# Kernel optimization log

Measured on AMD Instinct MI355X. Metric: run time of the kernel, lower is better.

Reference implementation:

```python
import jax, jax.numpy as jnp
import numpy as np

N = 10000      # nodes (= num_spatial_nodes)
E = 320000     # edges
IN = 4         # in_channels
HID = 256      # hidden_channels
H1, C1 = 4, 64 # conv1: heads, per-head out (hidden//heads)
EDIM = 1       # edge_feature_size
EPS = 1e-5


def _layernorm(x, g, b):
    mu = jnp.mean(x, axis=-1, keepdims=True)
    var = jnp.mean(jnp.square(x - mu), axis=-1, keepdims=True)
    return (x - mu) / jnp.sqrt(var + EPS) * g + b


def _gatv2(x, src, dst, ea, Wl, bl, Wr, br, We, att, bias, H, C, n):
    # PyG GATv2Conv: lin_l on source, lin_r on target, lin_edge on edge_attr
    xl = (x @ Wl + bl).reshape(n, H, C)
    xr = (x @ Wr + br).reshape(n, H, C)
    ee = (ea @ We).reshape(-1, H, C)
    m = jax.nn.leaky_relu(xl[src] + xr[dst] + ee, 0.2)   # [E', H, C]
    logit = jnp.einsum('ehc,hc->eh', m, att)             # [E', H]
    # segment softmax over incoming edges of each dst node
    mx = jax.ops.segment_max(logit, dst, num_segments=n)
    ex = jnp.exp(logit - mx[dst])
    den = jax.ops.segment_sum(ex, dst, num_segments=n)
    alpha = ex / den[dst]
    out = jax.ops.segment_sum(xl[src] * alpha[:, :, None], dst, num_segments=n)
    return out.reshape(n, H * C) + bias


def setup_inputs() -> dict:
    key = jax.random.key(0)
    ks = jax.random.split(key, 32)
    gl = lambda k, shape, fan: (jax.random.normal(k, shape, jnp.float32) / np.sqrt(fan)).astype(jnp.float32)
    inp = {}
    inp['x'] = jax.random.normal(ks[0], (N, IN), jnp.float32)
    inp['edge_index'] = jax.random.randint(ks[1], (2, E), 0, N, jnp.int32)
    inp['edge_attr'] = jax.random.normal(ks[2], (E, EDIM), jnp.float32)
    # conv1 (heads=4, out=64, concat -> 256)
    inp['Wl1'] = gl(ks[3], (IN, HID), IN);  inp['bl1'] = jnp.zeros((HID,), jnp.float32)
    inp['Wr1'] = gl(ks[4], (IN, HID), IN);  inp['br1'] = jnp.zeros((HID,), jnp.float32)
    inp['We1'] = gl(ks[5], (EDIM, HID), EDIM)
    inp['att1'] = gl(ks[6], (H1, C1), C1)
    inp['bias1'] = jnp.zeros((HID,), jnp.float32)
    inp['g1'] = jnp.ones((HID,), jnp.float32); inp['be1'] = jnp.zeros((HID,), jnp.float32)
    # conv2 (heads=1, out=256)
    inp['Wl2'] = gl(ks[7], (HID, HID), HID); inp['bl2'] = jnp.zeros((HID,), jnp.float32)
    inp['Wr2'] = gl(ks[8], (HID, HID), HID); inp['br2'] = jnp.zeros((HID,), jnp.float32)
    inp['We2'] = gl(ks[9], (EDIM, HID), EDIM)
    inp['att2'] = gl(ks[10], (1, HID), HID)
    inp['bias2'] = jnp.zeros((HID,), jnp.float32)
    inp['g2'] = jnp.ones((HID,), jnp.float32); inp['be2'] = jnp.zeros((HID,), jnp.float32)
    # policy head
    inp['Wp1'] = gl(ks[11], (HID, HID // 2), HID); inp['bp1'] = jnp.zeros((HID // 2,), jnp.float32)
    inp['Wp2'] = gl(ks[12], (HID // 2, IN), HID // 2); inp['bp2'] = jnp.zeros((IN,), jnp.float32)
    return inp


def reference(x, edge_index, edge_attr,
              Wl1, bl1, Wr1, br1, We1, att1, bias1, g1, be1,
              Wl2, bl2, Wr2, br2, We2, att2, bias2, g2, be2,
              Wp1, bp1, Wp2, bp2):
    src, dst = edge_index[0], edge_index[1]
    # add_self_loops with fill_value='mean': loop edge_attr = mean of incoming edge_attr
    deg = jax.ops.segment_sum(jnp.ones((E,), jnp.float32), dst, num_segments=N)
    loop_attr = jax.ops.segment_sum(edge_attr, dst, num_segments=N) / jnp.maximum(deg, 1.0)[:, None]
    ar = jnp.arange(N, dtype=src.dtype)
    src_a = jnp.concatenate([src, ar]); dst_a = jnp.concatenate([dst, ar])
    ea_a = jnp.concatenate([edge_attr, loop_attr], axis=0)
    h = _gatv2(x, src_a, dst_a, ea_a, Wl1, bl1, Wr1, br1, We1, att1, bias1, H1, C1, N)
    h = jax.nn.relu(_layernorm(h, g1, be1))
    h = _gatv2(h, src_a, dst_a, ea_a, Wl2, bl2, Wr2, br2, We2, att2, bias2, 1, HID, N)
    h = jax.nn.relu(_layernorm(h, g2, be2))
    logits = jax.nn.relu(h @ Wp1 + bp1) @ Wp2 + bp2   # [N, IN]
    return jax.nn.softmax(logits.reshape(1, -1), axis=1)
```

## Files before the change

### kernel.cpp

```cpp
#include <hip/hip_runtime.h>
#include <math.h>

#define N_NODES 10000
#define N_EDGES 320000
#define N_AUG   (N_EDGES + N_NODES)
#define CPK_CAP 330752
#define HID     256

typedef short short8 __attribute__((ext_vector_type(8)));
typedef float floatx16 __attribute__((ext_vector_type(16)));

static __device__ __forceinline__ unsigned bf16rne(float f) {
  unsigned u = __float_as_uint(f);
  return (u + 0x7FFFu + ((u >> 16) & 1u)) >> 16;
}

__global__ void k_deg(const int* __restrict__ dst, const float* __restrict__ ea,
                      int* __restrict__ deg, float* __restrict__ asum,
                      int* __restrict__ rank) {
  int e = blockIdx.x * blockDim.x + threadIdx.x;
  if (e < N_EDGES) {
    int d = dst[e];
    rank[e] = atomicAdd(&deg[d], 1);
    atomicAdd(&asum[d], ea[e]);
  }
}

__global__ void __launch_bounds__(256) k_scan(
    const int* __restrict__ deg, const float* __restrict__ asum,
    int* __restrict__ offs, float* __restrict__ lattr) {
  __shared__ int wsum[4];
  int t = threadIdx.x;
  int base = t * 40;
  int s = 0;
  for (int i = 0; i < 40; i++) {
    int n = base + i;
    if (n < N_NODES) s += deg[n] + 1;
  }
  int v = s;
  #pragma unroll
  for (int d = 1; d < 64; d <<= 1) {
    int u = __shfl_up(v, d);
    if ((t & 63) >= d) v += u;
  }
  if ((t & 63) == 63) wsum[t >> 6] = v;
  __syncthreads();
  int wb = 0;
  for (int i = 0; i < (t >> 6); i++) wb += wsum[i];
  int run = wb + v - s;
  for (int i = 0; i < 40; i++) {
    int n = base + i;
    if (n < N_NODES) {
      offs[n] = run;
      int d = deg[n];
      run += d + 1;
      lattr[n] = asum[n] / (float)max(d, 1);
    }
  }
  if (t == 255) offs[N_NODES] = wb + v;
}

__global__ void k_scatter(const int* __restrict__ src, const int* __restrict__ dst,
                          const float* __restrict__ ea, const float* __restrict__ lattr,
                          const int* __restrict__ offs, const int* __restrict__ rank,
                          int2* __restrict__ cpk) {
  int e = blockIdx.x * blockDim.x + threadIdx.x;
  if (e >= N_AUG) {
    if (e < CPK_CAP) cpk[e] = make_int2(0, 0);
    return;
  }
  int pos, s; float a;
  if (e < N_EDGES) {
    s = src[e];
    int d = dst[e];
    a = ea[e];
    pos = offs[d] + rank[e];
  } else {
    s = e - N_EDGES;
    a = lattr[s];
    pos = offs[s + 1] - 1;
  }
  cpk[pos] = make_int2(s, __float_as_int(a));
}

__global__ void __launch_bounds__(256) k_prep(
    const float* __restrict__ W1, const float* __restrict__ W2,
    const float* __restrict__ Wp1,
    unsigned short* __restrict__ Wt, unsigned short* __restrict__ Wp1t) {
  __shared__ float tile[32][33];
  int z = blockIdx.z;
  int kb = blockIdx.x * 32, nb = blockIdx.y * 32;
  int t = threadIdx.x;
  int tx = t & 31, ty = t >> 5;
  if (z < 2) {
    const float* W = z ? W2 : W1;
    int rowoff = z * 256;
    #pragma unroll
    for (int rep = 0; rep < 4; rep++)
      tile[ty + 8*rep][tx] = W[(kb + ty + 8*rep)*HID + nb + tx];
    __syncthreads();
    #pragma unroll
    for (int rep = 0; rep < 4; rep++) {
      int n = nb + ty + 8*rep;
      Wt[(rowoff + n)*256 + kb + tx] = (unsigned short)bf16rne(tile[tx][ty + 8*rep]);
    }
  } else {
    if (nb >= 128) return;
    #pragma unroll
    for (int rep = 0; rep < 4; rep++)
      tile[ty + 8*rep][tx] = Wp1[(kb + ty + 8*rep)*128 + nb + tx];
    __syncthreads();
    #pragma unroll
    for (int rep = 0; rep < 4; rep++) {
      int n = nb + ty + 8*rep;
      Wp1t[n*256 + kb + tx] = (unsigned short)bf16rne(tile[tx][ty + 8*rep]);
    }
  }
}

#define C1_EDGE(xs, av, l0, l1, l2, l3, p)                                              \
  {                                                                                     \
    l0 = fmaf(xs.x,wl0.x, fmaf(xs.y,wl1.x, fmaf(xs.z,wl2.x, fmaf(xs.w,wl3.x, blv.x)))); \
    l1 = fmaf(xs.x,wl0.y, fmaf(xs.y,wl1.y, fmaf(xs.z,wl2.y, fmaf(xs.w,wl3.y, blv.y)))); \
    l2 = fmaf(xs.x,wl0.z, fmaf(xs.y,wl1.z, fmaf(xs.z,wl2.z, fmaf(xs.w,wl3.z, blv.z)))); \
    l3 = fmaf(xs.x,wl0.w, fmaf(xs.y,wl1.w, fmaf(xs.z,wl2.w, fmaf(xs.w,wl3.w, blv.w)))); \
    float m0 = l0 + fmaf(av, we.x, r4.x); m0 = fmaxf(m0, 0.2f*m0);                      \
    float m1 = l1 + fmaf(av, we.y, r4.y); m1 = fmaxf(m1, 0.2f*m1);                      \
    float m2 = l2 + fmaf(av, we.z, r4.z); m2 = fmaxf(m2, 0.2f*m2);                      \
    float m3 = l3 + fmaf(av, we.w, r4.w); m3 = fmaxf(m3, 0.2f*m3);                      \
    p = m0*at.x + m1*at.y + m2*at.z + m3*at.w;                                          \
  }

#define C1_BODY8()                                                              \
  {                                                                             \
    float avA = __int_as_float(eA.y), avB = __int_as_float(eB.y);               \
    float avC = __int_as_float(eC.y), avD = __int_as_float(eD.y);               \
    float avE = __int_as_float(eE.y), avF = __int_as_float(eF.y);               \
    float avG = __int_as_float(eG.y), avH = __int_as_float(eH.y);               \
    float lA0,lA1,lA2,lA3,pA, lB0,lB1,lB2,lB3,pB;                               \
    float lC0,lC1,lC2,lC3,pC, lD0,lD1,lD2,lD3,pD;                               \
    float lE0,lE1,lE2,lE3,pE, lF0,lF1,lF2,lF3,pF;                               \
    float lG0,lG1,lG2,lG3,pG, lH0,lH1,lH2,lH3,pH;                               \
    C1_EDGE(xA, avA, lA0,lA1,lA2,lA3, pA);                                      \
    C1_EDGE(xB, avB, lB0,lB1,lB2,lB3, pB);                                      \
    C1_EDGE(xC, avC, lC0,lC1,lC2,lC3, pC);                                      \
    C1_EDGE(xD, avD, lD0,lD1,lD2,lD3, pD);                                      \
    C1_EDGE(xE, avE, lE0,lE1,lE2,lE3, pE);                                      \
    C1_EDGE(xF, avF, lF0,lF1,lF2,lF3, pF);                                      \
    C1_EDGE(xG, avG, lG0,lG1,lG2,lG3, pG);                                      \
    C1_EDGE(xH, avH, lH0,lH1,lH2,lH3, pH);                                      \
    float sAB = b1 ? pA : pB, kAB = b1 ? pB : pA;                               \
    float qAB = kAB + __shfl_xor(sAB, 1);                                       \
    float sCD = b1 ? pC : pD, kCD = b1 ? pD : pC;                               \
    float qCD = kCD + __shfl_xor(sCD, 1);                                       \
    float sEF = b1 ? pE : pF, kEF = b1 ? pF : pE;                               \
    float qEF = kEF + __shfl_xor(sEF, 1);                                       \
    float sGH = b1 ? pG : pH, kGH = b1 ? pH : pG;                               \
    float qGH = kGH + __shfl_xor(sGH, 1);                                       \
    float u0s = b2 ? qAB : qCD, u0k = b2 ? qCD : qAB;                           \
    float u0 = u0k + __shfl_xor(u0s, 2);                                        \
    float u1s = b2 ? qEF : qGH, u1k = b2 ? qGH : qEF;                           \
    float u1 = u1k + __shfl_xor(u1s, 2);                                        \
    float vvs = b4 ? u0 : u1, vvk = b4 ? u1 : u0;                               \
    float vv = vvk + __shfl_xor(vvs, 4);                                        \
    vv += __shfl_xor(vv, 8);                                                    \
    float exv = expf(vv);                                                       \
    float xAe = __shfl(exv, 0, 16), xBe = __shfl(exv, 1, 16);                   \
    float xCe = __shfl(exv, 2, 16), xDe = __shfl(exv, 3, 16);                   \
    float xEe = __shfl(exv, 4, 16), xFe = __shfl(exv, 5, 16);                   \
    float xGe = __shfl(exv, 6, 16), xHe = __shfl(exv, 7, 16);                   \
    D += ((xAe + xBe) + (xCe + xDe)) + ((xEe + xFe) + (xGe + xHe));             \
    a0 = fmaf(xDe, lD0, fmaf(xCe, lC0, fmaf(xBe, lB0, fmaf(xAe, lA0, a0))));    \
    a0 = fmaf(xHe, lH0, fmaf(xGe, lG0, fmaf(xFe, lF0, fmaf(xEe, lE0, a0))));    \
    a1 = fmaf(xDe, lD1, fmaf(xCe, lC1, fmaf(xBe, lB1, fmaf(xAe, lA1, a1))));    \
    a1 = fmaf(xHe, lH1, fmaf(xGe, lG1, fmaf(xFe, lF1, fmaf(xEe, lE1, a1))));    \
    a2 = fmaf(xDe, lD2, fmaf(xCe, lC2, fmaf(xBe, lB2, fmaf(xAe, lA2, a2))));    \
    a2 = fmaf(xHe, lH2, fmaf(xGe, lG2, fmaf(xFe, lF2, fmaf(xEe, lE2, a2))));    \
    a3 = fmaf(xDe, lD3, fmaf(xCe, lC3, fmaf(xBe, lB3, fmaf(xAe, lA3, a3))));    \
    a3 = fmaf(xHe, lH3, fmaf(xGe, lG3, fmaf(xFe, lF3, fmaf(xEe, lE3, a3))));    \
  }

__global__ void __launch_bounds__(256) k_conv1(
    const float* __restrict__ x,
    const float* __restrict__ Wl, const float* __restrict__ bl,
    const float* __restrict__ Wr, const float* __restrict__ br,
    const float* __restrict__ We, const float* __restrict__ att,
    const int* __restrict__ offs, const int2* __restrict__ cpk,
    const float* __restrict__ bias, const float* __restrict__ g,
    const float* __restrict__ be, uint2* __restrict__ h1b) {
  int t = threadIdx.x;
  int n = blockIdx.x * 4 + (t >> 6);
  int c = 4 * (t & 63);
  bool b1 = (t & 1) != 0, b2 = (t & 2) != 0, b4 = (t & 4) != 0;

  float4 wl0 = *(const float4*)&Wl[0*HID + c];
  float4 wl1 = *(const float4*)&Wl[1*HID + c];
  float4 wl2 = *(const float4*)&Wl[2*HID + c];
  float4 wl3 = *(const float4*)&Wl[3*HID + c];
  float4 blv = *(const float4*)&bl[c];
  float4 we  = *(const float4*)&We[c];
  float4 at  = *(const float4*)&att[c];

  float4 xn = *(const float4*)&x[n*4];
  float4 r4;
  {
    float4 wr0 = *(const float4*)&Wr[0*HID + c];
    float4 wr1 = *(const float4*)&Wr[1*HID + c];
    float4 wr2 = *(const float4*)&Wr[2*HID + c];
    float4 wr3 = *(const float4*)&Wr[3*HID + c];
    float4 brv = *(const float4*)&br[c];
    r4.x = fmaf(xn.x,wr0.x, fmaf(xn.y,wr1.x, fmaf(xn.z,wr2.x, fmaf(xn.w,wr3.x, brv.x))));
    r4.y = fmaf(xn.x,wr0.y, fmaf(xn.y,wr1.y, fmaf(xn.z,wr2.y, fmaf(xn.w,wr3.y, brv.y))));
    r4.z = fmaf(xn.x,wr0.z, fmaf(xn.y,wr1.z, fmaf(xn.z,wr2.z, fmaf(xn.w,wr3.z, brv.z))));
    r4.w = fmaf(xn.x,wr0.w, fmaf(xn.y,wr1.w, fmaf(xn.z,wr2.w, fmaf(xn.w,wr3.w, brv.w))));
  }

  int js = __builtin_amdgcn_readfirstlane(offs[n]);
  int je = __builtin_amdgcn_readfirstlane(offs[n+1]);

  float D = 0.f, a0 = 0.f, a1 = 0.f, a2 = 0.f, a3 = 0.f;

  int j = js;
  if (je - js >= 16) {
    int2 eA = cpk[j],   eB = cpk[j+1], eC = cpk[j+2], eD = cpk[j+3];
    int2 eE = cpk[j+4], eF = cpk[j+5], eG = cpk[j+6], eH = cpk[j+7];
    int2 fA = cpk[j+8],  fB = cpk[j+9],  fC = cpk[j+10], fD = cpk[j+11];
    int2 fE = cpk[j+12], fF = cpk[j+13], fG = cpk[j+14], fH = cpk[j+15];
    float4 xA = *(const float4*)&x[eA.x*4];
    float4 xB = *(const float4*)&x[eB.x*4];
    float4 xC = *(const float4*)&x[eC.x*4];
    float4 xD = *(const float4*)&x[eD.x*4];
    float4 xE = *(const float4*)&x[eE.x*4];
    float4 xF = *(const float4*)&x[eF.x*4];
    float4 xG = *(const float4*)&x[eG.x*4];
    float4 xH = *(const float4*)&x[eH.x*4];
    for (; j + 15 < je; j += 8) {
      float4 yA = *(const float4*)&x[fA.x*4];
      float4 yB = *(const float4*)&x[fB.x*4];
      float4 yC = *(const float4*)&x[fC.x*4];
      float4 yD = *(const float4*)&x[fD.x*4];
      float4 yE = *(const float4*)&x[fE.x*4];
      float4 yF = *(const float4*)&x[fF.x*4];
      float4 yG = *(const float4*)&x[fG.x*4];
      float4 yH = *(const float4*)&x[fH.x*4];
      int2 gA = cpk[j+16], gB = cpk[j+17], gC = cpk[j+18], gD = cpk[j+19];
      int2 gE = cpk[j+20], gF = cpk[j+21], gG = cpk[j+22], gH = cpk[j+23];
      C1_BODY8();
      eA = fA; eB = fB; eC = fC; eD = fD; eE = fE; eF = fF; eG = fG; eH = fH;
      fA = gA; fB = gB; fC = gC; fD = gD; fE = gE; fF = gF; fG = gG; fH = gH;
      xA = yA; xB = yB; xC = yC; xD = yD; xE = yE; xF = yF; xG = yG; xH = yH;
    }
    C1_BODY8();
    j += 8;
  }
  for (; j + 7 < je; j += 8) {
    int2 eA = cpk[j],   eB = cpk[j+1], eC = cpk[j+2], eD = cpk[j+3];
    int2 eE = cpk[j+4], eF = cpk[j+5], eG = cpk[j+6], eH = cpk[j+7];
    float4 xA = *(const float4*)&x[eA.x*4];
    float4 xB = *(const float4*)&x[eB.x*4];
    float4 xC = *(const float4*)&x[eC.x*4];
    float4 xD = *(const float4*)&x[eD.x*4];
    float4 xE = *(const float4*)&x[eE.x*4];
    float4 xF = *(const float4*)&x[eF.x*4];
    float4 xG = *(const float4*)&x[eG.x*4];
    float4 xH = *(const float4*)&x[eH.x*4];
    C1_BODY8();
  }
  for (; j < je; j++) {
    int2 eA = cpk[j];
    float4 xA = *(const float4*)&x[eA.x*4];
    float avA = __int_as_float(eA.y);
    float lA0,lA1,lA2,lA3,pA;
    C1_EDGE(xA, avA, lA0,lA1,lA2,lA3, pA);
    #pragma unroll
    for (int msk = 1; msk < 16; msk <<= 1) pA += __shfl_xor(pA, msk);
    float eAx = expf(pA);
    D += eAx;
    a0 = fmaf(eAx, lA0, a0);
    a1 = fmaf(eAx, lA1, a1);
    a2 = fmaf(eAx, lA2, a2);
    a3 = fmaf(eAx, lA3, a3);
  }

  float inv = 1.f / D;
  float4 b4v = *(const float4*)&bias[c];
  float o0 = fmaf(a0, inv, b4v.x);
  float o1 = fmaf(a1, inv, b4v.y);
  float o2 = fmaf(a2, inv, b4v.z);
  float o3 = fmaf(a3, inv, b4v.w);

  float s = o0 + o1 + o2 + o3;
  #pragma unroll
  for (int msk = 1; msk < 64; msk <<= 1) s += __shfl_xor(s, msk);
  float mu = s * (1.f / 256.f);
  float d0 = o0 - mu, d1 = o1 - mu, d2 = o2 - mu, d3 = o3 - mu;
  float sq = d0*d0 + d1*d1 + d2*d2 + d3*d3;
  #pragma unroll
  for (int msk = 1; msk < 64; msk <<= 1) sq += __shfl_xor(sq, msk);
  float rstd = rsqrtf(sq * (1.f / 256.f) + 1e-5f);
  float4 g4  = *(const float4*)&g[c];
  float4 be4 = *(const float4*)&be[c];
  float oy0 = fmaxf(fmaf(d0 * rstd, g4.x, be4.x), 0.f);
  float oy1 = fmaxf(fmaf(d1 * rstd, g4.y, be4.y), 0.f);
  float oy2 = fmaxf(fmaf(d2 * rstd, g4.z, be4.z), 0.f);
  float oy3 = fmaxf(fmaf(d3 * rstd, g4.w, be4.w), 0.f);
  uint2 pk;
  pk.x = bf16rne(oy0) | (bf16rne(oy1) << 16);
  pk.y = bf16rne(oy2) | (bf16rne(oy3) << 16);
  h1b[n*64 + (t & 63)] = pk;
}

#define C2_LOAD(q, xs)                                  \
  float4 xs;                                            \
  xs.x = __uint_as_float(q.x << 16);                    \
  xs.y = __uint_as_float(q.x & 0xFFFF0000u);            \
  xs.z = __uint_as_float(q.y << 16);                    \
  xs.w = __uint_as_float(q.y & 0xFFFF0000u);

#define C2_EDGE(xs, av, p)                                           \
  {                                                                  \
    float m0 = xs.x + fmaf(av, we.x, r4.x); m0 = fmaxf(m0, 0.2f*m0); \
    float m1 = xs.y + fmaf(av, we.y, r4.y); m1 = fmaxf(m1, 0.2f*m1); \
    float m2 = xs.z + fmaf(av, we.z, r4.z); m2 = fmaxf(m2, 0.2f*m2); \
    float m3 = xs.w + fmaf(av, we.w, r4.w); m3 = fmaxf(m3, 0.2f*m3); \
    p = m0*at.x + m1*at.y + m2*at.z + m3*at.w;                       \
  }

#define C2_PROC8()                                                              \
  {                                                                             \
    C2_LOAD(q0, xs0); C2_LOAD(q1, xs1); C2_LOAD(q2, xs2); C2_LOAD(q3, xs3);     \
    C2_LOAD(q4, xs4); C2_LOAD(q5, xs5); C2_LOAD(q6, xs6); C2_LOAD(q7, xs7);     \
    float av0 = __int_as_float(e0.y), av1 = __int_as_float(e1.y);               \
    float av2 = __int_as_float(e2.y), av3 = __int_as_float(e3.y);               \
    float av4 = __int_as_float(e4.y), av5 = __int_as_float(e5.y);               \
    float av6 = __int_as_float(e6.y), av7 = __int_as_float(e7.y);               \
    float p0,p1,p2,p3,p4,p5,p6,p7;                                              \
    C2_EDGE(xs0, av0, p0); C2_EDGE(xs1, av1, p1);                               \
    C2_EDGE(xs2, av2, p2); C2_EDGE(xs3, av3, p3);                               \
    C2_EDGE(xs4, av4, p4); C2_EDGE(xs5, av5, p5);                               \
    C2_EDGE(xs6, av6, p6); C2_EDGE(xs7, av7, p7);                               \
    float sAB = b1 ? p0 : p1, kAB = b1 ? p1 : p0;                               \
    float qAB = kAB + __shfl_xor(sAB, 1);                                       \
    float sCD = b1 ? p2 : p3, kCD = b1 ? p3 : p2;                               \
    float qCD = kCD + __shfl_xor(sCD, 1);                                       \
    float sEF = b1 ? p4 : p5, kEF = b1 ? p5 : p4;                               \
    float qEF = kEF + __shfl_xor(sEF, 1);                                       \
    float sGH = b1 ? p6 : p7, kGH = b1 ? p7 : p6;                               \
    float qGH = kGH + __shfl_xor(sGH, 1);                                       \
    float u0s = b2 ? qAB : qCD, u0k = b2 ? qCD : qAB;                           \
    float u0 = u0k + __shfl_xor(u0s, 2);                                        \
    float u1s = b2 ? qEF : qGH, u1k = b2 ? qGH : qEF;                           \
    float u1 = u1k + __shfl_xor(u1s, 2);                                        \
    float vvs = b4 ? u0 : u1, vvk = b4 ? u1 : u0;                               \
    float vv = vvk + __shfl_xor(vvs, 4);                                        \
    vv += __shfl_xor(vv, 8);                                                    \
    vv += __shfl_xor(vv, 16);                                                   \
    vv += __shfl_xor(vv, 32);                                                   \
    float exv = expf(vv);                                                       \
    float x0 = __shfl(exv, 0), x1 = __shfl(exv, 1);                             \
    float x2 = __shfl(exv, 2), x3 = __shfl(exv, 3);                             \
    float x4 = __shfl(exv, 4), x5 = __shfl(exv, 5);                             \
    float x6 = __shfl(exv, 6), x7 = __shfl(exv, 7);                             \
    D += ((x0 + x1) + (x2 + x3)) + ((x4 + x5) + (x6 + x7));                     \
    a0 = fmaf(x3, xs3.x, fmaf(x2, xs2.x, fmaf(x1, xs1.x, fmaf(x0, xs0.x, a0))));\
    a0 = fmaf(x7, xs7.x, fmaf(x6, xs6.x, fmaf(x5, xs5.x, fmaf(x4, xs4.x, a0))));\
    a1 = fmaf(x3, xs3.y, fmaf(x2, xs2.y, fmaf(x1, xs1.y, fmaf(x0, xs0.y, a1))));\
    a1 = fmaf(x7, xs7.y, fmaf(x6, xs6.y, fmaf(x5, xs5.y, fmaf(x4, xs4.y, a1))));\
    a2 = fmaf(x3, xs3.z, fmaf(x2, xs2.z, fmaf(x1, xs1.z, fmaf(x0, xs0.z, a2))));\
    a2 = fmaf(x7, xs7.z, fmaf(x6, xs6.z, fmaf(x5, xs5.z, fmaf(x4, xs4.z, a2))));\
    a3 = fmaf(x3, xs3.w, fmaf(x2, xs2.w, fmaf(x1, xs1.w, fmaf(x0, xs0.w, a3))));\
    a3 = fmaf(x7, xs7.w, fmaf(x6, xs6.w, fmaf(x5, xs5.w, fmaf(x4, xs4.w, a3))));\
  }

__global__ void __launch_bounds__(256) k_conv2(
    const uint2* __restrict__ xlb, const float* __restrict__ xr,
    const int* __restrict__ offs, const int2* __restrict__ cpk,
    const float* __restrict__ We, const float* __restrict__ att,
    const float* __restrict__ bias, const float* __restrict__ g,
    const float* __restrict__ be, uint2* __restrict__ h2b) {
  int t = threadIdx.x;
  int n = blockIdx.x * 4 + (t >> 6);
  int lane = t & 63;
  int c = 4 * lane;
  bool b1 = (t & 1) != 0, b2 = (t & 2) != 0, b4 = (t & 4) != 0;
  float4 r4 = *(const float4*)&xr[n*HID + c];
  float4 we = *(const float4*)&We[c];
  float4 at = *(const float4*)&att[c];
  int js = __builtin_amdgcn_readfirstlane(offs[n]);
  int je = __builtin_amdgcn_readfirstlane(offs[n+1]);

  float D = 0.f, a0 = 0.f, a1 = 0.f, a2 = 0.f, a3 = 0.f;

  int j = js;
  if (je - js >= 16) {
    int2 e0 = cpk[j],   e1 = cpk[j+1], e2 = cpk[j+2], e3 = cpk[j+3];
    int2 e4 = cpk[j+4], e5 = cpk[j+5], e6 = cpk[j+6], e7 = cpk[j+7];
    int2 f0 = cpk[j+8],  f1 = cpk[j+9],  f2 = cpk[j+10], f3 = cpk[j+11];
    int2 f4 = cpk[j+12], f5 = cpk[j+13], f6 = cpk[j+14], f7 = cpk[j+15];
    uint2 q0 = xlb[e0.x*64 + lane];
    uint2 q1 = xlb[e1.x*64 + lane];
    uint2 q2 = xlb[e2.x*64 + lane];
    uint2 q3 = xlb[e3.x*64 + lane];
    uint2 q4 = xlb[e4.x*64 + lane];
    uint2 q5 = xlb[e5.x*64 + lane];
    uint2 q6 = xlb[e6.x*64 + lane];
    uint2 q7 = xlb[e7.x*64 + lane];
    for (; j + 15 < je; j += 8) {
      uint2 r0 = xlb[f0.x*64 + lane];
      uint2 r1 = xlb[f1.x*64 + lane];
      uint2 r2 = xlb[f2.x*64 + lane];
      uint2 r3 = xlb[f3.x*64 + lane];
      uint2 r4_ = xlb[f4.x*64 + lane];
      uint2 r5 = xlb[f5.x*64 + lane];
      uint2 r6 = xlb[f6.x*64 + lane];
      uint2 r7 = xlb[f7.x*64 + lane];
      int2 g0 = cpk[j+16], g1 = cpk[j+17], g2 = cpk[j+18], g3 = cpk[j+19];
      int2 g4 = cpk[j+20], g5 = cpk[j+21], g6 = cpk[j+22], g7 = cpk[j+23];
      C2_PROC8();
      e0 = f0; e1 = f1; e2 = f2; e3 = f3; e4 = f4; e5 = f5; e6 = f6; e7 = f7;
      f0 = g0; f1 = g1; f2 = g2; f3 = g3; f4 = g4; f5 = g5; f6 = g6; f7 = g7;
      q0 = r0; q1 = r1; q2 = r2; q3 = r3; q4 = r4_; q5 = r5; q6 = r6; q7 = r7;
    }
    C2_PROC8();
    j += 8;
  }
  for (; j + 7 < je; j += 8) {
    int2 e0 = cpk[j],   e1 = cpk[j+1], e2 = cpk[j+2], e3 = cpk[j+3];
    int2 e4 = cpk[j+4], e5 = cpk[j+5], e6 = cpk[j+6], e7 = cpk[j+7];
    uint2 q0 = xlb[e0.x*64 + lane];
    uint2 q1 = xlb[e1.x*64 + lane];
    uint2 q2 = xlb[e2.x*64 + lane];
    uint2 q3 = xlb[e3.x*64 + lane];
    uint2 q4 = xlb[e4.x*64 + lane];
    uint2 q5 = xlb[e5.x*64 + lane];
    uint2 q6 = xlb[e6.x*64 + lane];
    uint2 q7 = xlb[e7.x*64 + lane];
    C2_PROC8();
  }
  for (; j < je; j++) {
    int2 e0 = cpk[j];
    float av0 = __int_as_float(e0.y);
    uint2 q0 = xlb[e0.x*64 + lane];
    C2_LOAD(q0, xs0);
    float p0;
    C2_EDGE(xs0, av0, p0);
    #pragma unroll
    for (int msk = 1; msk < 64; msk <<= 1) p0 += __shfl_xor(p0, msk);
    float x0 = expf(p0);
    D += x0;
    a0 = fmaf(x0, xs0.x, a0);
    a1 = fmaf(x0, xs0.y, a1);
    a2 = fmaf(x0, xs0.z, a2);
    a3 = fmaf(x0, xs0.w, a3);
  }

  float inv = 1.f / D;
  float4 b4v = *(const float4*)&bias[c];
  float o0 = fmaf(a0, inv, b4v.x);
  float o1 = fmaf(a1, inv, b4v.y);
  float o2 = fmaf(a2, inv, b4v.z);
  float o3 = fmaf(a3, inv, b4v.w);

  float s = o0 + o1 + o2 + o3;
  #pragma unroll
  for (int msk = 1; msk < 64; msk <<= 1) s += __shfl_xor(s, msk);
  float mu = s * (1.f / 256.f);
  float d0 = o0 - mu, d1 = o1 - mu, d2 = o2 - mu, d3 = o3 - mu;
  float sq = d0*d0 + d1*d1 + d2*d2 + d3*d3;
  #pragma unroll
  for (int msk = 1; msk < 64; msk <<= 1) sq += __shfl_xor(sq, msk);
  float rstd = rsqrtf(sq * (1.f / 256.f) + 1e-5f);
  float4 g4  = *(const float4*)&g[c];
  float4 be4 = *(const float4*)&be[c];
  float oy0 = fmaxf(fmaf(d0 * rstd, g4.x, be4.x), 0.f);
  float oy1 = fmaxf(fmaf(d1 * rstd, g4.y, be4.y), 0.f);
  float oy2 = fmaxf(fmaf(d2 * rstd, g4.z, be4.z), 0.f);
  float oy3 = fmaxf(fmaf(d3 * rstd, g4.w, be4.w), 0.f);
  uint2 pk;
  pk.x = bf16rne(oy0) | (bf16rne(oy1) << 16);
  pk.y = bf16rne(oy2) | (bf16rne(oy3) << 16);
  h2b[n*64 + lane] = pk;
}

__global__ void __launch_bounds__(256) k_gemm_dual(
    const unsigned short* __restrict__ h1b, const unsigned short* __restrict__ Wt,
    const float* __restrict__ b1, const float* __restrict__ b2,
    unsigned short* __restrict__ O1b, float* __restrict__ O2) {
  __shared__ unsigned short A_lds[64][72];
  __shared__ unsigned short W_lds[128][72];
  int t = threadIdx.x;
  int r0 = blockIdx.x * 64;
  int nb0 = blockIdx.y * 128;
  int l = t & 63;
  int wave = t >> 6;
  int wr = wave >> 1, wc = wave & 1;

  floatx16 acc[2] = {{0}, {0}};

  int sar = t >> 2, sak = (t & 3) * 16;
  int arow = min(r0 + sar, N_NODES - 1);
  int swn = t >> 1, swk = (t & 1) * 32;
  const unsigned short* Wrow = &Wt[(nb0 + swn) * 256];

  for (int kb = 0; kb < 256; kb += 64) {
    uint4 av0 = *(const uint4*)&h1b[arow*256 + kb + sak];
    uint4 av1 = *(const uint4*)&h1b[arow*256 + kb + sak + 8];
    uint4 wv0 = *(const uint4*)&Wrow[kb + swk];
    uint4 wv1 = *(const uint4*)&Wrow[kb + swk + 8];
    uint4 wv2 = *(const uint4*)&Wrow[kb + swk + 16];
    uint4 wv3 = *(const uint4*)&Wrow[kb + swk + 24];
    __syncthreads();
    *(uint4*)&A_lds[sar][sak]     = av0;
    *(uint4*)&A_lds[sar][sak + 8] = av1;
    *(uint4*)&W_lds[swn][swk]      = wv0;
    *(uint4*)&W_lds[swn][swk +  8] = wv1;
    *(uint4*)&W_lds[swn][swk + 16] = wv2;
    *(uint4*)&W_lds[swn][swk + 24] = wv3;
    __syncthreads();
    #pragma unroll
    for (int ks = 0; ks < 64; ks += 16) {
      short8 af  = *(const short8*)&A_lds[wr*32 + (l & 31)][ks + 8*(l >> 5)];
      short8 bf0 = *(const short8*)&W_lds[wc*64      + (l & 31)][ks + 8*(l >> 5)];
      short8 bf1 = *(const short8*)&W_lds[wc*64 + 32 + (l & 31)][ks + 8*(l >> 5)];
      acc[0] = __builtin_amdgcn_mfma_f32_32x32x16_bf16(af, bf0, acc[0], 0, 0, 0);
      acc[1] = __builtin_amdgcn_mfma_f32_32x32x16_bf16(af, bf1, acc[1], 0, 0, 0);
    }
  }

  bool isO1 = (nb0 < 256);
  #pragma unroll
  for (int tile = 0; tile < 2; tile++) {
    int col = nb0 + wc*64 + tile*32 + (l & 31);
    float bias = isO1 ? b1[col] : b2[col - 256];
    #pragma unroll
    for (int reg = 0; reg < 16; reg++) {
      int row = (reg & 3) + 8*(reg >> 2) + 4*(l >> 5);
      int r = r0 + wr*32 + row;
      if (r < N_NODES) {
        float v = acc[tile][reg] + bias;
        if (isO1) O1b[r*256 + col] = (unsigned short)bf16rne(v);
        else      O2[r*256 + (col - 256)] = v;
      }
    }
  }
}

__global__ void __launch_bounds__(256) k_policy(
    const unsigned short* __restrict__ h2b, const unsigned short* __restrict__ Wp1t,
    const float* __restrict__ bp1, const float* __restrict__ Wp2,
    const float* __restrict__ bp2, float* __restrict__ elg, float* __restrict__ tot) {
  __shared__ __align__(16) char smembuf[64 * 132 * 4];
  unsigned short* A_lds = (unsigned short*)smembuf;
  unsigned short* W_lds = (unsigned short*)(smembuf + 64*72*2);
  float* hidl = (float*)smembuf;
  __shared__ float wred[4];
  int t = threadIdx.x;
  int r0 = blockIdx.x * 64;
  int l = t & 63;
  int wave = t >> 6;
  int wr = wave >> 1, wc = wave & 1;

  floatx16 acc[2] = {{0}, {0}};

  int sar = t >> 2, sak = (t & 3) * 16;
  int arow = min(r0 + sar, N_NODES - 1);
  int swn = t >> 1, swk = (t & 1) * 32;
  const unsigned short* Wrow = &Wp1t[swn * 256];

  for (int kb = 0; kb < 256; kb += 64) {
    uint4 av0 = *(const uint4*)&h2b[arow*256 + kb + sak];
    uint4 av1 = *(const uint4*)&h2b[arow*256 + kb + sak + 8];
    uint4 wv0 = *(const uint4*)&Wrow[kb + swk];
    uint4 wv1 = *(const uint4*)&Wrow[kb + swk + 8];
    uint4 wv2 = *(const uint4*)&Wrow[kb + swk + 16];
    uint4 wv3 = *(const uint4*)&Wrow[kb + swk + 24];
    __syncthreads();
    *(uint4*)&A_lds[sar*72 + sak]     = av0;
    *(uint4*)&A_lds[sar*72 + sak + 8] = av1;
    *(uint4*)&W_lds[swn*72 + swk]      = wv0;
    *(uint4*)&W_lds[swn*72 + swk +  8] = wv1;
    *(uint4*)&W_lds[swn*72 + swk + 16] = wv2;
    *(uint4*)&W_lds[swn*72 + swk + 24] = wv3;
    __syncthreads();
    #pragma unroll
    for (int ks = 0; ks < 64; ks += 16) {
      short8 af  = *(const short8*)&A_lds[(wr*32 + (l & 31))*72 + ks + 8*(l >> 5)];
      short8 bf0 = *(const short8*)&W_lds[(wc*64      + (l & 31))*72 + ks + 8*(l >> 5)];
      short8 bf1 = *(const short8*)&W_lds[(wc*64 + 32 + (l & 31))*72 + ks + 8*(l >> 5)];
      acc[0] = __builtin_amdgcn_mfma_f32_32x32x16_bf16(af, bf0, acc[0], 0, 0, 0);
      acc[1] = __builtin_amdgcn_mfma_f32_32x32x16_bf16(af, bf1, acc[1], 0, 0, 0);
    }
  }
  __syncthreads();
  #pragma unroll
  for (int tile = 0; tile < 2; tile++) {
    int col = wc*64 + tile*32 + (l & 31);
    float bias = bp1[col];
    #pragma unroll
    for (int reg = 0; reg < 16; reg++) {
      int row = (reg & 3) + 8*(reg >> 2) + 4*(l >> 5) + wr*32;
      hidl[row*132 + col] = fmaxf(acc[tile][reg] + bias, 0.f);
    }
  }
  __syncthreads();
  int nl = t >> 2, i = t & 3;
  float s = bp2[i];
  for (int k = 0; k < 128; k += 4) {
    float4 hv = *(const float4*)&hidl[nl*132 + k];
    s = fmaf(hv.x, Wp2[(k+0)*4 + i],
        fmaf(hv.y, Wp2[(k+1)*4 + i],
        fmaf(hv.z, Wp2[(k+2)*4 + i],
        fmaf(hv.w, Wp2[(k+3)*4 + i], s))));
  }
  int n = r0 + nl;
  float esum = 0.f;
  if (n < N_NODES) {
    float e = expf(s);
    elg[n*4 + i] = e;
    esum = e;
  }
  #pragma unroll
  for (int msk = 1; msk < 64; msk <<= 1) esum += __shfl_xor(esum, msk);
  if ((t & 63) == 0) wred[t >> 6] = esum;
  __syncthreads();
  if (t == 0) atomicAdd(tot, (wred[0] + wred[1]) + (wred[2] + wred[3]));
}

__global__ void __launch_bounds__(1024) k_sm_final(const float* __restrict__ elg,
                                                   const float* __restrict__ tot,
                                                   float* __restrict__ out) {
  int i = blockIdx.x * 1024 + threadIdx.x;
  float inv = 1.f / tot[0];
  if (i < N_NODES * 4) out[i] = elg[i] * inv;
}

extern "C" void kernel_launch(void* const* d_in, const int* in_sizes, int n_in,
                              void* d_out, int out_size, void* d_ws, size_t ws_size,
                              hipStream_t stream) {
  const float* x    = (const float*)d_in[0];
  const int*   ei   = (const int*)  d_in[1];
  const float* ea   = (const float*)d_in[2];
  const float* Wl1  = (const float*)d_in[3];
  const float* bl1  = (const float*)d_in[4];
  const float* Wr1  = (const float*)d_in[5];
  const float* br1  = (const float*)d_in[6];
  const float* We1  = (const float*)d_in[7];
  const float* att1 = (const float*)d_in[8];
  const float* bias1= (const float*)d_in[9];
  const float* g1   = (const float*)d_in[10];
  const float* be1  = (const float*)d_in[11];
  const float* Wl2  = (const float*)d_in[12];
  const float* bl2  = (const float*)d_in[13];
  const float* Wr2  = (const float*)d_in[14];
  const float* br2  = (const float*)d_in[15];
  const float* We2  = (const float*)d_in[16];
  const float* att2 = (const float*)d_in[17];
  const float* bias2= (const float*)d_in[18];
  const float* g2   = (const float*)d_in[19];
  const float* be2  = (const float*)d_in[20];
  const float* Wp1  = (const float*)d_in[21];
  const float* bp1  = (const float*)d_in[22];
  const float* Wp2  = (const float*)d_in[23];
  const float* bp2  = (const float*)d_in[24];
  float* out = (float*)d_out;

  const int* srcp = ei;
  const int* dstp = ei + N_EDGES;

  int*   deg    = (int*)d_ws;
  float* asum   = (float*)(deg + 10240);
  float* tot    = asum + 10240;
  int*   offs   = (int*)(tot + 16);
  float* lattr  = (float*)(offs + 10240);
  int*   rank   = (int*)(lattr + 10240);
  int2*  cpk    = (int2*)(rank + 320192);
  unsigned short* h1b = (unsigned short*)(cpk + CPK_CAP);
  unsigned short* h2b = h1b;
  unsigned short* xl2bf = h1b + 2560000;
  float* xr2    = (float*)(xl2bf + 2560000);
  float* elg    = xr2 + 2560000;
  unsigned short* Wt   = (unsigned short*)(elg + 40960);
  unsigned short* Wp1t = Wt + 512*256;

  hipMemsetAsync(deg, 0, (2 * 10240 + 16) * sizeof(int), stream);

  k_prep   <<<dim3(8, 8, 3), 256, 0, stream>>>(Wl2, Wr2, Wp1, Wt, Wp1t);
  k_deg    <<<(N_EDGES + 255)/256, 256, 0, stream>>>(dstp, ea, deg, asum, rank);
  k_scan   <<<1, 256, 0, stream>>>(deg, asum, offs, lattr);
  k_scatter<<<(CPK_CAP + 255)/256, 256, 0, stream>>>(srcp, dstp, ea, lattr, offs,
                                                     rank, cpk);
  k_conv1  <<<N_NODES/4, 256, 0, stream>>>(x, Wl1, bl1, Wr1, br1, We1, att1,
                                           offs, cpk, bias1, g1, be1, (uint2*)h1b);
  k_gemm_dual<<<dim3(157, 4), 256, 0, stream>>>(h1b, Wt, bl2, br2, xl2bf, xr2);
  k_conv2  <<<N_NODES/4, 256, 0, stream>>>((const uint2*)xl2bf, xr2, offs, cpk,
                                           We2, att2, bias2, g2, be2, (uint2*)h2b);
  k_policy <<<157, 256, 0, stream>>>(h2b, Wp1t, bp1, Wp2, bp2, elg, tot);
  k_sm_final<<<40, 1024, 0, stream>>>(elg, tot, out);
}
```

Measured before the change: 287.9 us.

## Fuse degree count with weight prep, pack atomics, store xr2 as bf16

```diff
diff --git a/kernel.cpp b/kernel.cpp
--- a/kernel.cpp
+++ b/kernel.cpp
@@ -15,19 +15,58 @@
   return (u + 0x7FFFu + ((u >> 16) & 1u)) >> 16;
 }
 
-__global__ void k_deg(const int* __restrict__ dst, const float* __restrict__ ea,
-                      int* __restrict__ deg, float* __restrict__ asum,
-                      int* __restrict__ rank) {
-  int e = blockIdx.x * blockDim.x + threadIdx.x;
-  if (e < N_EDGES) {
+__global__ void __launch_bounds__(256) k_front(
+    const int* __restrict__ dst, const float* __restrict__ ea,
+    unsigned long long* __restrict__ pdeg, int* __restrict__ rank,
+    const float* __restrict__ W1, const float* __restrict__ W2,
+    const float* __restrict__ Wp1,
+    unsigned short* __restrict__ Wt, unsigned short* __restrict__ Wp1t) {
+  __shared__ float tile[32][33];
+  int bi = blockIdx.x;
+  int t = threadIdx.x;
+  if (bi < 1250) {
+    int e = bi * 256 + t;
     int d = dst[e];
-    rank[e] = atomicAdd(&deg[d], 1);
-    atomicAdd(&asum[d], ea[e]);
+    int fx = __float2int_rn(ea[e] * 262144.0f);
+    unsigned long long pk = 0x100000000ull
+                          + (unsigned long long)(unsigned)(fx + 2097152);
+    unsigned long long old = atomicAdd(&pdeg[d], pk);
+    rank[e] = (int)(old >> 32);
+    return;
+  }
+  int pb = bi - 1250;
+  int z = pb >> 6;
+  int rem = pb & 63;
+  int kb = (rem & 7) * 32, nb = (rem >> 3) * 32;
+  int tx = t & 31, ty = t >> 5;
+  if (z < 2) {
+    const float* W = z ? W2 : W1;
+    int rowoff = z * 256;
+    #pragma unroll
+    for (int rep = 0; rep < 4; rep++)
+      tile[ty + 8*rep][tx] = W[(kb + ty + 8*rep)*HID + nb + tx];
+    __syncthreads();
+    #pragma unroll
+    for (int rep = 0; rep < 4; rep++) {
+      int n = nb + ty + 8*rep;
+      Wt[(rowoff + n)*256 + kb + tx] = (unsigned short)bf16rne(tile[tx][ty + 8*rep]);
+    }
+  } else {
+    if (nb >= 128) return;
+    #pragma unroll
+    for (int rep = 0; rep < 4; rep++)
+      tile[ty + 8*rep][tx] = Wp1[(kb + ty + 8*rep)*128 + nb + tx];
+    __syncthreads();
+    #pragma unroll
+    for (int rep = 0; rep < 4; rep++) {
+      int n = nb + ty + 8*rep;
+      Wp1t[n*256 + kb + tx] = (unsigned short)bf16rne(tile[tx][ty + 8*rep]);
+    }
   }
 }
 
 __global__ void __launch_bounds__(256) k_scan(
-    const int* __restrict__ deg, const float* __restrict__ asum,
+    const unsigned long long* __restrict__ pdeg,
     int* __restrict__ offs, float* __restrict__ lattr) {
   __shared__ int wsum[4];
   int t = threadIdx.x;
@@ -35,7 +74,7 @@
   int s = 0;
   for (int i = 0; i < 40; i++) {
     int n = base + i;
-    if (n < N_NODES) s += deg[n] + 1;
+    if (n < N_NODES) s += (int)(pdeg[n] >> 32) + 1;
   }
   int v = s;
   #pragma unroll
@@ -52,9 +91,12 @@
     int n = base + i;
     if (n < N_NODES) {
       offs[n] = run;
-      int d = deg[n];
+      unsigned long long pv = pdeg[n];
+      int d = (int)(pv >> 32);
       run += d + 1;
-      lattr[n] = asum[n] / (float)max(d, 1);
+      int lower = (int)(pv & 0xFFFFFFFFull);
+      float asum = (float)(lower - d * 2097152) * (1.f / 262144.f);
+      lattr[n] = asum / (float)max(d, 1);
     }
   }
   if (t == 255) offs[N_NODES] = wb + v;
@@ -81,41 +123,6 @@
     pos = offs[s + 1] - 1;
   }
   cpk[pos] = make_int2(s, __float_as_int(a));
-}
-
-__global__ void __launch_bounds__(256) k_prep(
-    const float* __restrict__ W1, const float* __restrict__ W2,
-    const float* __restrict__ Wp1,
-    unsigned short* __restrict__ Wt, unsigned short* __restrict__ Wp1t) {
-  __shared__ float tile[32][33];
-  int z = blockIdx.z;
-  int kb = blockIdx.x * 32, nb = blockIdx.y * 32;
-  int t = threadIdx.x;
-  int tx = t & 31, ty = t >> 5;
-  if (z < 2) {
-    const float* W = z ? W2 : W1;
-    int rowoff = z * 256;
-    #pragma unroll
-    for (int rep = 0; rep < 4; rep++)
-      tile[ty + 8*rep][tx] = W[(kb + ty + 8*rep)*HID + nb + tx];
-    __syncthreads();
-    #pragma unroll
-    for (int rep = 0; rep < 4; rep++) {
-      int n = nb + ty + 8*rep;
-      Wt[(rowoff + n)*256 + kb + tx] = (unsigned short)bf16rne(tile[tx][ty + 8*rep]);
-    }
-  } else {
-    if (nb >= 128) return;
-    #pragma unroll
-    for (int rep = 0; rep < 4; rep++)
-      tile[ty + 8*rep][tx] = Wp1[(kb + ty + 8*rep)*128 + nb + tx];
-    __syncthreads();
-    #pragma unroll
-    for (int rep = 0; rep < 4; rep++) {
-      int n = nb + ty + 8*rep;
-      Wp1t[n*256 + kb + tx] = (unsigned short)bf16rne(tile[tx][ty + 8*rep]);
-    }
-  }
 }
 
 #define C1_EDGE(xs, av, l0, l1, l2, l3, p)                                              \
@@ -373,7 +380,7 @@
   }
 
 __global__ void __launch_bounds__(256) k_conv2(
-    const uint2* __restrict__ xlb, const float* __restrict__ xr,
+    const uint2* __restrict__ xlb, const uint2* __restrict__ xrb,
     const int* __restrict__ offs, const int2* __restrict__ cpk,
     const float* __restrict__ We, const float* __restrict__ att,
     const float* __restrict__ bias, const float* __restrict__ g,
@@ -383,7 +390,8 @@
   int lane = t & 63;
   int c = 4 * lane;
   bool b1 = (t & 1) != 0, b2 = (t & 2) != 0, b4 = (t & 4) != 0;
-  float4 r4 = *(const float4*)&xr[n*HID + c];
+  uint2 rq = xrb[n*64 + lane];
+  C2_LOAD(rq, r4);
   float4 we = *(const float4*)&We[c];
   float4 at = *(const float4*)&att[c];
   int js = __builtin_amdgcn_readfirstlane(offs[n]);
@@ -485,7 +493,7 @@
 __global__ void __launch_bounds__(256) k_gemm_dual(
     const unsigned short* __restrict__ h1b, const unsigned short* __restrict__ Wt,
     const float* __restrict__ b1, const float* __restrict__ b2,
-    unsigned short* __restrict__ O1b, float* __restrict__ O2) {
+    unsigned short* __restrict__ O1b, unsigned short* __restrict__ O2b) {
   __shared__ unsigned short A_lds[64][72];
   __shared__ unsigned short W_lds[128][72];
   int t = threadIdx.x;
@@ -539,7 +547,7 @@
       if (r < N_NODES) {
         float v = acc[tile][reg] + bias;
         if (isO1) O1b[r*256 + col] = (unsigned short)bf16rne(v);
-        else      O2[r*256 + (col - 256)] = v;
+        else      O2b[r*256 + (col - 256)] = (unsigned short)bf16rne(v);
       }
     }
   }
@@ -667,33 +675,33 @@
   const int* srcp = ei;
   const int* dstp = ei + N_EDGES;
 
-  int*   deg    = (int*)d_ws;
-  float* asum   = (float*)(deg + 10240);
-  float* tot    = asum + 10240;
-  int*   offs   = (int*)(tot + 16);
-  float* lattr  = (float*)(offs + 10240);
-  int*   rank   = (int*)(lattr + 10240);
-  int2*  cpk    = (int2*)(rank + 320192);
-  unsigned short* h1b = (unsigned short*)(cpk + CPK_CAP);
-  unsigned short* h2b = h1b;
+  unsigned long long* pdeg = (unsigned long long*)d_ws;
+  float* tot   = (float*)(pdeg + 10240);
+  int*   offs  = (int*)(tot + 16);
+  float* lattr = (float*)(offs + 10240);
+  int*   rank  = (int*)(lattr + 10240);
+  int2*  cpk   = (int2*)(rank + 320192);
+  unsigned short* h1b   = (unsigned short*)(cpk + CPK_CAP);
+  unsigned short* h2b   = h1b;
   unsigned short* xl2bf = h1b + 2560000;
-  float* xr2    = (float*)(xl2bf + 2560000);
-  float* elg    = xr2 + 2560000;
+  unsigned short* xr2b  = xl2bf + 2560000;
+  float* elg   = (float*)(xr2b + 2560000);
   unsigned short* Wt   = (unsigned short*)(elg + 40960);
   unsigned short* Wp1t = Wt + 512*256;
 
-  hipMemsetAsync(deg, 0, (2 * 10240 + 16) * sizeof(int), stream);
-
-  k_prep   <<<dim3(8, 8, 3), 256, 0, stream>>>(Wl2, Wr2, Wp1, Wt, Wp1t);
-  k_deg    <<<(N_EDGES + 255)/256, 256, 0, stream>>>(dstp, ea, deg, asum, rank);
-  k_scan   <<<1, 256, 0, stream>>>(deg, asum, offs, lattr);
+  hipMemsetAsync(pdeg, 0, 10240 * 8 + 64, stream);
+
+  k_front  <<<1250 + 192, 256, 0, stream>>>(dstp, ea, pdeg, rank,
+                                            Wl2, Wr2, Wp1, Wt, Wp1t);
+  k_scan   <<<1, 256, 0, stream>>>(pdeg, offs, lattr);
   k_scatter<<<(CPK_CAP + 255)/256, 256, 0, stream>>>(srcp, dstp, ea, lattr, offs,
                                                      rank, cpk);
   k_conv1  <<<N_NODES/4, 256, 0, stream>>>(x, Wl1, bl1, Wr1, br1, We1, att1,
                                            offs, cpk, bias1, g1, be1, (uint2*)h1b);
-  k_gemm_dual<<<dim3(157, 4), 256, 0, stream>>>(h1b, Wt, bl2, br2, xl2bf, xr2);
-  k_conv2  <<<N_NODES/4, 256, 0, stream>>>((const uint2*)xl2bf, xr2, offs, cpk,
-                                           We2, att2, bias2, g2, be2, (uint2*)h2b);
+  k_gemm_dual<<<dim3(157, 4), 256, 0, stream>>>(h1b, Wt, bl2, br2, xl2bf, xr2b);
+  k_conv2  <<<N_NODES/4, 256, 0, stream>>>((const uint2*)xl2bf, (const uint2*)xr2b,
+                                           offs, cpk, We2, att2, bias2, g2, be2,
+                                           (uint2*)h2b);
   k_policy <<<157, 256, 0, stream>>>(h2b, Wp1t, bp1, Wp2, bp2, elg, tot);
   k_sm_final<<<40, 1024, 0, stream>>>(elg, tot, out);
 }
```

Measured after the change: 252.5 us, median of 2. 12.3% less time.
